# Kernel tuning notes

Measured on AMD Instinct MI355X. Metric: run time of the kernel, lower is better.

Reference implementation:

```python
import jax, jax.numpy as jnp
import numpy as np

NEG_FILL = -10000.0  # matches masked_fill_(mask, -10000.0)


def setup_inputs() -> dict:
    key0 = jax.random.key(0)
    kq, kk, kv, km = jax.random.split(key0, 4)
    B, H, S, D = 2, 16, 2048, 64
    query = jax.random.normal(kq, (B, H, S, D), dtype=jnp.float32)
    key = jax.random.normal(kk, (B, H, S, D), dtype=jnp.float32)
    value = jax.random.normal(kv, (B, H, S, D), dtype=jnp.float32)
    # key-padding mask [B, S]; True = position is masked out
    mask = jax.random.randint(km, (B, S), 0, 2).astype(jnp.bool_)
    return {"query": query, "key": key, "value": value, "mask": mask}


def reference(query, key, value, mask):
    # scaled dot-product attention: [B,H,S,D] x [B,H,S,D] -> [B,H,S,S]
    scale = 1.0 / jnp.sqrt(jnp.asarray(query.shape[-1], query.dtype))
    scores = jnp.einsum('bhqd,bhkd->bhqk', query, key) * scale
    # mask [B,S] -> broadcast over heads and query positions as [B,1,1,S]
    scores = jnp.where(mask[:, None, None, :], jnp.asarray(NEG_FILL, scores.dtype), scores)
    attn = jax.nn.softmax(scores, axis=-1)
    # dropout probs are 0 (eval-mode identity)
    out = jnp.einsum('bhqk,bhkd->bhqd', attn, value)
    return out
```

## Files before the change

kernel.cpp:

```cpp
#include <hip/hip_runtime.h>
#include <hip/hip_bf16.h>
#include <stdint.h>

namespace {

constexpr int Bb = 2;
constexpr int Hh = 16;
constexpr int Ss = 2048;
constexpr int Dd = 64;
constexpr int KT = 64;
constexpr int NT = Ss / KT;
constexpr int TILE_BYTES = KT * Dd * 2;
constexpr int BH_BYTES = NT * TILE_BYTES;
constexpr size_t KPRE_BYTES = (size_t)Bb * Hh * Ss * Dd * 2;
constexpr size_t VPRE_OFF = KPRE_BYTES;
constexpr size_t MASK_OFF = 2 * KPRE_BYTES;
constexpr size_t WS_NEED = MASK_OFF + (size_t)Bb * NT * 8;
constexpr int NIT = 16;
constexpr int IT_BYTES = 2 * TILE_BYTES;

typedef __bf16 bf16x8 __attribute__((ext_vector_type(8)));
typedef float floatx4 __attribute__((ext_vector_type(4)));

typedef __attribute__((address_space(1))) const unsigned int guint;
typedef __attribute__((address_space(3))) unsigned int luint;

__device__ __forceinline__ void g2lds16(const void* g, void* l) {
  __builtin_amdgcn_global_load_lds((guint*)g, (luint*)l, 16, 0, 0);
}

__global__ __launch_bounds__(256) void preprocess3(
    const float* __restrict__ K, const float* __restrict__ V,
    const int* __restrict__ mask, uint8_t* __restrict__ ws)
{
  const int tid = threadIdx.x;
  const int kt = blockIdx.x;
  const int bh = blockIdx.y;

  if (blockIdx.z == 0) {
    const int c = tid & 7;
#pragma unroll
    for (int half = 0; half < 2; ++half) {
      const int row = (tid >> 3) + half * 32;
      const float4* src = (const float4*)(K + ((size_t)bh * 2048 + kt * 64 + row) * 64 + c * 8);
      const float4 a = src[0], b2 = src[1];
      bf16x8 pk;
      pk[0] = (__bf16)a.x;  pk[1] = (__bf16)a.y;  pk[2] = (__bf16)a.z;  pk[3] = (__bf16)a.w;
      pk[4] = (__bf16)b2.x; pk[5] = (__bf16)b2.y; pk[6] = (__bf16)b2.z; pk[7] = (__bf16)b2.w;
      uint8_t* dst = ws + (size_t)bh * BH_BYTES + kt * TILE_BYTES + row * 128 + ((c ^ (row & 7)) << 4);
      *(bf16x8*)dst = pk;
    }
    if (bh == 0 && kt < 16) {
      const int i = kt * 256 + tid;
      const int bb = i >> 11, key = i & 2047;
      const unsigned long long bal = __ballot(mask[bb * 2048 + key] != 0);
      if ((key & 63) == 0)
        ((unsigned long long*)(ws + MASK_OFF))[bb * NT + (key >> 6)] = bal;
    }
    return;
  }

  __shared__ float Vsh[64 * 68];
#pragma unroll
  for (int i = 0; i < 4; ++i) {
    const int vt = tid + 256 * i;
    const int row = vt >> 4, c4 = vt & 15;
    const float4 v4 = *(const float4*)(V + ((size_t)bh * 2048 + kt * 64 + row) * 64 + c4 * 4);
    *(float4*)&Vsh[row * 68 + c4 * 4] = v4;
  }
  __syncthreads();
  {
    const int c16 = tid & 7;
    const int s2 = c16 & 1, q = c16 >> 1;
    const int k0 = 32 * s2 + 4 * q;
#pragma unroll
    for (int half = 0; half < 2; ++half) {
      const int d = (tid >> 3) + half * 32;
      bf16x8 pv;
#pragma unroll
      for (int j = 0; j < 4; ++j) {
        pv[j]     = (__bf16)Vsh[(k0 + j) * 68 + d];
        pv[4 + j] = (__bf16)Vsh[(k0 + 16 + j) * 68 + d];
      }
      uint8_t* dst = ws + VPRE_OFF + (size_t)bh * BH_BYTES + kt * TILE_BYTES + d * 128 + ((c16 ^ (d & 7)) << 4);
      *(bf16x8*)dst = pv;
    }
  }
}

#define NEGM (-14426.950408889634f)

__global__ __launch_bounds__(256, 2) void attn_fused6(
    const float* __restrict__ Q, const uint8_t* __restrict__ ws,
    float* __restrict__ Out)
{
  const int tid  = threadIdx.x;
  const int wave = tid >> 6;
  const int lane = tid & 63;
  const int ln   = lane & 15;
  const int quad = lane >> 4;

  const int bh   = blockIdx.x;
  const int qblk = blockIdx.y;
  const int b    = bh >> 4;

  const float* Qb = Q + (size_t)bh * Ss * Dd;
  float*       Ob = Out + (size_t)bh * Ss * Dd;
  const uint8_t* Kpre = ws + (size_t)bh * BH_BYTES;
  const uint8_t* Vpre = ws + VPRE_OFF + (size_t)bh * BH_BYTES;
  const unsigned long long* Mbits = (const unsigned long long*)(ws + MASK_OFF) + b * NT;

  __shared__ __align__(16) __bf16 Klds[2][128 * Dd];
  __shared__ __align__(16) __bf16 Vlds[2][128 * Dd];

  const int q0A = qblk * 128 + wave * 32;
  const int q0B = q0A + 16;

  const float QS = 0.125f * 1.44269504088896340736f;
  bf16x8 aqA0, aqA1, aqB0, aqB1;
  {
    const float* qpA = Qb + (size_t)(q0A + ln) * Dd + quad * 8;
    const float* qpB = Qb + (size_t)(q0B + ln) * Dd + quad * 8;
#pragma unroll
    for (int j = 0; j < 8; ++j) {
      aqA0[j] = (__bf16)(qpA[j] * QS);
      aqA1[j] = (__bf16)(qpA[32 + j] * QS);
      aqB0[j] = (__bf16)(qpB[j] * QS);
      aqB1[j] = (__bf16)(qpB[32 + j] * QS);
    }
  }

  floatx4 oA[4], oB[4];
  floatx4 laccA = (floatx4){0.f, 0.f, 0.f, 0.f};
  floatx4 laccB = (floatx4){0.f, 0.f, 0.f, 0.f};
#pragma unroll
  for (int nd = 0; nd < 4; ++nd) {
    oA[nd] = (floatx4){0.f, 0.f, 0.f, 0.f};
    oB[nd] = (floatx4){0.f, 0.f, 0.f, 0.f};
  }

  const int swz0 = (quad ^ (ln & 7)) << 4;
  const int swz1 = ((quad + 4) ^ (ln & 7)) << 4;
  const int soff = wave * 4096 + lane * 16;

#pragma unroll
  for (int i = 0; i < 4; ++i) {
    g2lds16(Kpre + soff + i * 1024, (uint8_t*)Klds[0] + soff + i * 1024);
    g2lds16(Vpre + soff + i * 1024, (uint8_t*)Vlds[0] + soff + i * 1024);
  }

  for (int kt2 = 0; kt2 < NIT; ++kt2) {
    const int cur = kt2 & 1;
    __syncthreads();

    if (kt2 + 1 < NIT) {
      const uint8_t* kg = Kpre + (kt2 + 1) * IT_BYTES;
      const uint8_t* vg = Vpre + (kt2 + 1) * IT_BYTES;
      uint8_t* kl = (uint8_t*)Klds[cur ^ 1];
      uint8_t* vl = (uint8_t*)Vlds[cur ^ 1];
#pragma unroll
      for (int i = 0; i < 4; ++i) {
        g2lds16(kg + soff + i * 1024, kl + soff + i * 1024);
        g2lds16(vg + soff + i * 1024, vl + soff + i * 1024);
      }
    }

    const unsigned long long mb0 = Mbits[2 * kt2];
    const unsigned long long mb1 = Mbits[2 * kt2 + 1];
    floatx4 biasC[8];
#pragma unroll
    for (int sub = 0; sub < 8; ++sub) {
      const unsigned long long mbx = (sub & 4) ? mb1 : mb0;
      const uint32_t bits = (uint32_t)(mbx >> ((sub & 3) * 16 + quad * 4));
#pragma unroll
      for (int r = 0; r < 4; ++r)
        biasC[sub][r] = ((bits >> r) & 1) ? NEGM : 0.f;
    }

    floatx4 sA[8], sB[8];
#pragma unroll
    for (int sub = 0; sub < 8; ++sub) {
      const uint8_t* krow = (const uint8_t*)Klds[cur] + (sub >> 2) * 8192 + ((sub & 3) * 16 + ln) * 128;
      const bf16x8 bk0 = *(const bf16x8*)(krow + swz0);
      const bf16x8 bk1 = *(const bf16x8*)(krow + swz1);
      floatx4 cA = biasC[sub];
      cA = __builtin_amdgcn_mfma_f32_16x16x32_bf16(bk0, aqA0, cA, 0, 0, 0);
      cA = __builtin_amdgcn_mfma_f32_16x16x32_bf16(bk1, aqA1, cA, 0, 0, 0);
      sA[sub] = cA;
      floatx4 cB = biasC[sub];
      cB = __builtin_amdgcn_mfma_f32_16x16x32_bf16(bk0, aqB0, cB, 0, 0, 0);
      cB = __builtin_amdgcn_mfma_f32_16x16x32_bf16(bk1, aqB1, cB, 0, 0, 0);
      sB[sub] = cB;
    }

    bf16x8 bpA[4], bpB[4];
#pragma unroll
    for (int sub = 0; sub < 8; ++sub) {
      const int pair = sub >> 1, u = sub & 1;
#pragma unroll
      for (int r = 0; r < 4; ++r) {
        const float pA = __builtin_amdgcn_exp2f(sA[sub][r]);
        const float pB = __builtin_amdgcn_exp2f(sB[sub][r]);
        laccA[r] += pA;
        laccB[r] += pB;
        bpA[pair][u * 4 + r] = (__bf16)pA;
        bpB[pair][u * 4 + r] = (__bf16)pB;
      }
    }

#pragma unroll
    for (int nd = 0; nd < 4; ++nd) {
#pragma unroll
      for (int T = 0; T < 2; ++T) {
        const uint8_t* vrow = (const uint8_t*)Vlds[cur] + T * 8192 + (nd * 16 + ln) * 128;
#pragma unroll
        for (int s2 = 0; s2 < 2; ++s2) {
          const bf16x8 w = *(const bf16x8*)(vrow + (((quad * 2 + s2) ^ (ln & 7)) << 4));
          const int pair = T * 2 + s2;
          oA[nd] = __builtin_amdgcn_mfma_f32_16x16x32_bf16(w, bpA[pair], oA[nd], 0, 0, 0);
          oB[nd] = __builtin_amdgcn_mfma_f32_16x16x32_bf16(w, bpB[pair], oB[nd], 0, 0, 0);
        }
      }
    }
  }

  float lA = (laccA[0] + laccA[1]) + (laccA[2] + laccA[3]);
  float lB = (laccB[0] + laccB[1]) + (laccB[2] + laccB[3]);
  lA += __shfl_xor(lA, 16); lA += __shfl_xor(lA, 32);
  lB += __shfl_xor(lB, 16); lB += __shfl_xor(lB, 32);
  const float iA = 1.0f / lA, iB = 1.0f / lB;
#pragma unroll
  for (int nd = 0; nd < 4; ++nd) {
    float4 wv;
    wv.x = oA[nd][0] * iA; wv.y = oA[nd][1] * iA;
    wv.z = oA[nd][2] * iA; wv.w = oA[nd][3] * iA;
    *(float4*)(Ob + (size_t)(q0A + ln) * Dd + nd * 16 + quad * 4) = wv;
    wv.x = oB[nd][0] * iB; wv.y = oB[nd][1] * iB;
    wv.z = oB[nd][2] * iB; wv.w = oB[nd][3] * iB;
    *(float4*)(Ob + (size_t)(q0B + ln) * Dd + nd * 16 + quad * 4) = wv;
  }
}

}

extern "C" void kernel_launch(void* const* d_in, const int* in_sizes, int n_in,
                              void* d_out, int out_size, void* d_ws, size_t ws_size,
                              hipStream_t stream) {
  const float* Q   = (const float*)d_in[0];
  const float* K   = (const float*)d_in[1];
  const float* V   = (const float*)d_in[2];
  const int*  mask = (const int*)d_in[3];
  float* Out = (float*)d_out;

  preprocess3<<<dim3(32, 32, 2), 256, 0, stream>>>(K, V, mask, (uint8_t*)d_ws);
  attn_fused6<<<dim3(Bb * Hh, Ss / 128), 256, 0, stream>>>(Q, (const uint8_t*)d_ws, Out);
  (void)ws_size; (void)in_sizes; (void)n_in; (void)out_size;
}
```

Measured before the change: 135.9 us.

## Process 64 query rows per wave with two-wave blocks for K/V reuse

```diff
diff --git a/kernel.cpp b/kernel.cpp
--- a/kernel.cpp
+++ b/kernel.cpp
@@ -15,7 +15,6 @@
 constexpr size_t KPRE_BYTES = (size_t)Bb * Hh * Ss * Dd * 2;
 constexpr size_t VPRE_OFF = KPRE_BYTES;
 constexpr size_t MASK_OFF = 2 * KPRE_BYTES;
-constexpr size_t WS_NEED = MASK_OFF + (size_t)Bb * NT * 8;
 constexpr int NIT = 16;
 constexpr int IT_BYTES = 2 * TILE_BYTES;
 
@@ -90,7 +89,7 @@
 
 #define NEGM (-14426.950408889634f)
 
-__global__ __launch_bounds__(256, 2) void attn_fused6(
+__global__ __launch_bounds__(128, 1) void attn_fused7(
     const float* __restrict__ Q, const uint8_t* __restrict__ ws,
     float* __restrict__ Out)
 {
@@ -113,40 +112,38 @@
   __shared__ __align__(16) __bf16 Klds[2][128 * Dd];
   __shared__ __align__(16) __bf16 Vlds[2][128 * Dd];
 
-  const int q0A = qblk * 128 + wave * 32;
-  const int q0B = q0A + 16;
+  const int qbase = qblk * 128 + wave * 64;
 
   const float QS = 0.125f * 1.44269504088896340736f;
-  bf16x8 aqA0, aqA1, aqB0, aqB1;
-  {
-    const float* qpA = Qb + (size_t)(q0A + ln) * Dd + quad * 8;
-    const float* qpB = Qb + (size_t)(q0B + ln) * Dd + quad * 8;
+  bf16x8 aq0[4], aq1[4];
+#pragma unroll
+  for (int X = 0; X < 4; ++X) {
+    const float* qp = Qb + (size_t)(qbase + X * 16 + ln) * Dd + quad * 8;
 #pragma unroll
     for (int j = 0; j < 8; ++j) {
-      aqA0[j] = (__bf16)(qpA[j] * QS);
-      aqA1[j] = (__bf16)(qpA[32 + j] * QS);
-      aqB0[j] = (__bf16)(qpB[j] * QS);
-      aqB1[j] = (__bf16)(qpB[32 + j] * QS);
-    }
-  }
-
-  floatx4 oA[4], oB[4];
-  floatx4 laccA = (floatx4){0.f, 0.f, 0.f, 0.f};
-  floatx4 laccB = (floatx4){0.f, 0.f, 0.f, 0.f};
-#pragma unroll
-  for (int nd = 0; nd < 4; ++nd) {
-    oA[nd] = (floatx4){0.f, 0.f, 0.f, 0.f};
-    oB[nd] = (floatx4){0.f, 0.f, 0.f, 0.f};
+      aq0[X][j] = (__bf16)(qp[j] * QS);
+      aq1[X][j] = (__bf16)(qp[32 + j] * QS);
+    }
+  }
+
+  floatx4 o[4][4];
+  floatx4 lacc[4];
+#pragma unroll
+  for (int X = 0; X < 4; ++X) {
+    lacc[X] = (floatx4){0.f, 0.f, 0.f, 0.f};
+#pragma unroll
+    for (int nd = 0; nd < 4; ++nd) o[X][nd] = (floatx4){0.f, 0.f, 0.f, 0.f};
   }
 
   const int swz0 = (quad ^ (ln & 7)) << 4;
   const int swz1 = ((quad + 4) ^ (ln & 7)) << 4;
-  const int soff = wave * 4096 + lane * 16;
-
-#pragma unroll
-  for (int i = 0; i < 4; ++i) {
-    g2lds16(Kpre + soff + i * 1024, (uint8_t*)Klds[0] + soff + i * 1024);
-    g2lds16(Vpre + soff + i * 1024, (uint8_t*)Vlds[0] + soff + i * 1024);
+
+  const int soff = tid * 16;
+
+#pragma unroll
+  for (int i = 0; i < 8; ++i) {
+    g2lds16(Kpre + soff + i * 2048, (uint8_t*)Klds[0] + soff + i * 2048);
+    g2lds16(Vpre + soff + i * 2048, (uint8_t*)Vlds[0] + soff + i * 2048);
   }
 
   for (int kt2 = 0; kt2 < NIT; ++kt2) {
@@ -159,85 +156,86 @@
       uint8_t* kl = (uint8_t*)Klds[cur ^ 1];
       uint8_t* vl = (uint8_t*)Vlds[cur ^ 1];
 #pragma unroll
-      for (int i = 0; i < 4; ++i) {
-        g2lds16(kg + soff + i * 1024, kl + soff + i * 1024);
-        g2lds16(vg + soff + i * 1024, vl + soff + i * 1024);
+      for (int i = 0; i < 8; ++i) {
+        g2lds16(kg + soff + i * 2048, kl + soff + i * 2048);
+        g2lds16(vg + soff + i * 2048, vl + soff + i * 2048);
       }
     }
 
     const unsigned long long mb0 = Mbits[2 * kt2];
     const unsigned long long mb1 = Mbits[2 * kt2 + 1];
-    floatx4 biasC[8];
-#pragma unroll
-    for (int sub = 0; sub < 8; ++sub) {
-      const unsigned long long mbx = (sub & 4) ? mb1 : mb0;
-      const uint32_t bits = (uint32_t)(mbx >> ((sub & 3) * 16 + quad * 4));
-#pragma unroll
-      for (int r = 0; r < 4; ++r)
-        biasC[sub][r] = ((bits >> r) & 1) ? NEGM : 0.f;
-    }
-
-    floatx4 sA[8], sB[8];
-#pragma unroll
-    for (int sub = 0; sub < 8; ++sub) {
-      const uint8_t* krow = (const uint8_t*)Klds[cur] + (sub >> 2) * 8192 + ((sub & 3) * 16 + ln) * 128;
-      const bf16x8 bk0 = *(const bf16x8*)(krow + swz0);
-      const bf16x8 bk1 = *(const bf16x8*)(krow + swz1);
-      floatx4 cA = biasC[sub];
-      cA = __builtin_amdgcn_mfma_f32_16x16x32_bf16(bk0, aqA0, cA, 0, 0, 0);
-      cA = __builtin_amdgcn_mfma_f32_16x16x32_bf16(bk1, aqA1, cA, 0, 0, 0);
-      sA[sub] = cA;
-      floatx4 cB = biasC[sub];
-      cB = __builtin_amdgcn_mfma_f32_16x16x32_bf16(bk0, aqB0, cB, 0, 0, 0);
-      cB = __builtin_amdgcn_mfma_f32_16x16x32_bf16(bk1, aqB1, cB, 0, 0, 0);
-      sB[sub] = cB;
-    }
-
-    bf16x8 bpA[4], bpB[4];
-#pragma unroll
-    for (int sub = 0; sub < 8; ++sub) {
-      const int pair = sub >> 1, u = sub & 1;
-#pragma unroll
-      for (int r = 0; r < 4; ++r) {
-        const float pA = __builtin_amdgcn_exp2f(sA[sub][r]);
-        const float pB = __builtin_amdgcn_exp2f(sB[sub][r]);
-        laccA[r] += pA;
-        laccB[r] += pB;
-        bpA[pair][u * 4 + r] = (__bf16)pA;
-        bpB[pair][u * 4 + r] = (__bf16)pB;
-      }
-    }
-
-#pragma unroll
-    for (int nd = 0; nd < 4; ++nd) {
-#pragma unroll
-      for (int T = 0; T < 2; ++T) {
+
+#pragma unroll
+    for (int T = 0; T < 2; ++T) {
+      const unsigned long long mbx = T ? mb1 : mb0;
+
+      floatx4 biasC[4];
+#pragma unroll
+      for (int s4 = 0; s4 < 4; ++s4) {
+        const uint32_t bits = (uint32_t)(mbx >> (s4 * 16 + quad * 4));
+#pragma unroll
+        for (int r = 0; r < 4; ++r)
+          biasC[s4][r] = ((bits >> r) & 1) ? NEGM : 0.f;
+      }
+
+      floatx4 s[4][4];
+#pragma unroll
+      for (int s4 = 0; s4 < 4; ++s4) {
+        const uint8_t* krow = (const uint8_t*)Klds[cur] + T * 8192 + (s4 * 16 + ln) * 128;
+        const bf16x8 bk0 = *(const bf16x8*)(krow + swz0);
+        const bf16x8 bk1 = *(const bf16x8*)(krow + swz1);
+#pragma unroll
+        for (int X = 0; X < 4; ++X) {
+          floatx4 c = biasC[s4];
+          c = __builtin_amdgcn_mfma_f32_16x16x32_bf16(bk0, aq0[X], c, 0, 0, 0);
+          c = __builtin_amdgcn_mfma_f32_16x16x32_bf16(bk1, aq1[X], c, 0, 0, 0);
+          s[s4][X] = c;
+        }
+      }
+
+      bf16x8 bp[4][2];
+#pragma unroll
+      for (int s4 = 0; s4 < 4; ++s4) {
+        const int s2 = s4 >> 1, u = s4 & 1;
+#pragma unroll
+        for (int X = 0; X < 4; ++X) {
+#pragma unroll
+          for (int r = 0; r < 4; ++r) {
+            const float p = __builtin_amdgcn_exp2f(s[s4][X][r]);
+            lacc[X][r] += p;
+            bp[X][s2][u * 4 + r] = (__bf16)p;
+          }
+        }
+      }
+
+#pragma unroll
+      for (int nd = 0; nd < 4; ++nd) {
         const uint8_t* vrow = (const uint8_t*)Vlds[cur] + T * 8192 + (nd * 16 + ln) * 128;
 #pragma unroll
         for (int s2 = 0; s2 < 2; ++s2) {
           const bf16x8 w = *(const bf16x8*)(vrow + (((quad * 2 + s2) ^ (ln & 7)) << 4));
-          const int pair = T * 2 + s2;
-          oA[nd] = __builtin_amdgcn_mfma_f32_16x16x32_bf16(w, bpA[pair], oA[nd], 0, 0, 0);
-          oB[nd] = __builtin_amdgcn_mfma_f32_16x16x32_bf16(w, bpB[pair], oB[nd], 0, 0, 0);
+#pragma unroll
+          for (int X = 0; X < 4; ++X)
+            o[X][nd] = __builtin_amdgcn_mfma_f32_16x16x32_bf16(w, bp[X][s2], o[X][nd], 0, 0, 0);
         }
       }
     }
   }
 
-  float lA = (laccA[0] + laccA[1]) + (laccA[2] + laccA[3]);
-  float lB = (laccB[0] + laccB[1]) + (laccB[2] + laccB[3]);
-  lA += __shfl_xor(lA, 16); lA += __shfl_xor(lA, 32);
-  lB += __shfl_xor(lB, 16); lB += __shfl_xor(lB, 32);
-  const float iA = 1.0f / lA, iB = 1.0f / lB;
-#pragma unroll
-  for (int nd = 0; nd < 4; ++nd) {
-    float4 wv;
-    wv.x = oA[nd][0] * iA; wv.y = oA[nd][1] * iA;
-    wv.z = oA[nd][2] * iA; wv.w = oA[nd][3] * iA;
-    *(float4*)(Ob + (size_t)(q0A + ln) * Dd + nd * 16 + quad * 4) = wv;
-    wv.x = oB[nd][0] * iB; wv.y = oB[nd][1] * iB;
-    wv.z = oB[nd][2] * iB; wv.w = oB[nd][3] * iB;
-    *(float4*)(Ob + (size_t)(q0B + ln) * Dd + nd * 16 + quad * 4) = wv;
+#pragma unroll
+  for (int X = 0; X < 4; ++X) {
+    float l = (lacc[X][0] + lacc[X][1]) + (lacc[X][2] + lacc[X][3]);
+    l += __shfl_xor(l, 16);
+    l += __shfl_xor(l, 32);
+    const float inv = 1.0f / l;
+    float* obX = Ob + (size_t)(qbase + X * 16 + ln) * Dd;
+#pragma unroll
+    for (int nd = 0; nd < 4; ++nd) {
+      float4 wv;
+      wv.x = o[X][nd][0] * inv; wv.y = o[X][nd][1] * inv;
+      wv.z = o[X][nd][2] * inv; wv.w = o[X][nd][3] * inv;
+      *(float4*)(obX + nd * 16 + quad * 4) = wv;
+    }
   }
 }
 
@@ -253,6 +251,6 @@
   float* Out = (float*)d_out;
 
   preprocess3<<<dim3(32, 32, 2), 256, 0, stream>>>(K, V, mask, (uint8_t*)d_ws);
-  attn_fused6<<<dim3(Bb * Hh, Ss / 128), 256, 0, stream>>>(Q, (const uint8_t*)d_ws, Out);
+  attn_fused7<<<dim3(Bb * Hh, Ss / 128), 128, 0, stream>>>(Q, (const uint8_t*)d_ws, Out);
   (void)ws_size; (void)in_sizes; (void)n_in; (void)out_size;
 }
```

Result: slower. 145.2 us (+6.8%).

## Halve key tile per iteration, raise occupancy, compute row sums via MFMA

Applied to the files above, without the earlier changes.

```diff
diff --git a/kernel.cpp b/kernel.cpp
--- a/kernel.cpp
+++ b/kernel.cpp
@@ -15,9 +15,6 @@
 constexpr size_t KPRE_BYTES = (size_t)Bb * Hh * Ss * Dd * 2;
 constexpr size_t VPRE_OFF = KPRE_BYTES;
 constexpr size_t MASK_OFF = 2 * KPRE_BYTES;
-constexpr size_t WS_NEED = MASK_OFF + (size_t)Bb * NT * 8;
-constexpr int NIT = 16;
-constexpr int IT_BYTES = 2 * TILE_BYTES;
 
 typedef __bf16 bf16x8 __attribute__((ext_vector_type(8)));
 typedef float floatx4 __attribute__((ext_vector_type(4)));
@@ -90,7 +87,7 @@
 
 #define NEGM (-14426.950408889634f)
 
-__global__ __launch_bounds__(256, 2) void attn_fused6(
+__global__ __launch_bounds__(256, 4) void attn_fused8(
     const float* __restrict__ Q, const uint8_t* __restrict__ ws,
     float* __restrict__ Out)
 {
@@ -110,8 +107,8 @@
   const uint8_t* Vpre = ws + VPRE_OFF + (size_t)bh * BH_BYTES;
   const unsigned long long* Mbits = (const unsigned long long*)(ws + MASK_OFF) + b * NT;
 
-  __shared__ __align__(16) __bf16 Klds[2][128 * Dd];
-  __shared__ __align__(16) __bf16 Vlds[2][128 * Dd];
+  __shared__ __align__(16) __bf16 Klds[2][KT * Dd];
+  __shared__ __align__(16) __bf16 Vlds[2][KT * Dd];
 
   const int q0A = qblk * 128 + wave * 32;
   const int q0B = q0A + 16;
@@ -130,9 +127,13 @@
     }
   }
 
+  bf16x8 ones;
+#pragma unroll
+  for (int j = 0; j < 8; ++j) ones[j] = (__bf16)1.0f;
+
   floatx4 oA[4], oB[4];
-  floatx4 laccA = (floatx4){0.f, 0.f, 0.f, 0.f};
-  floatx4 laccB = (floatx4){0.f, 0.f, 0.f, 0.f};
+  floatx4 clA = (floatx4){0.f, 0.f, 0.f, 0.f};
+  floatx4 clB = (floatx4){0.f, 0.f, 0.f, 0.f};
 #pragma unroll
   for (int nd = 0; nd < 4; ++nd) {
     oA[nd] = (floatx4){0.f, 0.f, 0.f, 0.f};
@@ -141,46 +142,43 @@
 
   const int swz0 = (quad ^ (ln & 7)) << 4;
   const int swz1 = ((quad + 4) ^ (ln & 7)) << 4;
-  const int soff = wave * 4096 + lane * 16;
-
-#pragma unroll
-  for (int i = 0; i < 4; ++i) {
-    g2lds16(Kpre + soff + i * 1024, (uint8_t*)Klds[0] + soff + i * 1024);
-    g2lds16(Vpre + soff + i * 1024, (uint8_t*)Vlds[0] + soff + i * 1024);
-  }
-
-  for (int kt2 = 0; kt2 < NIT; ++kt2) {
-    const int cur = kt2 & 1;
+  const int soff0 = wave * 2048 + lane * 16;
+  const int soff1 = soff0 + 1024;
+
+  g2lds16(Kpre + soff0, (uint8_t*)Klds[0] + soff0);
+  g2lds16(Vpre + soff0, (uint8_t*)Vlds[0] + soff0);
+  g2lds16(Kpre + soff1, (uint8_t*)Klds[0] + soff1);
+  g2lds16(Vpre + soff1, (uint8_t*)Vlds[0] + soff1);
+
+  for (int kt = 0; kt < NT; ++kt) {
+    const int cur = kt & 1;
     __syncthreads();
 
-    if (kt2 + 1 < NIT) {
-      const uint8_t* kg = Kpre + (kt2 + 1) * IT_BYTES;
-      const uint8_t* vg = Vpre + (kt2 + 1) * IT_BYTES;
+    if (kt + 1 < NT) {
+      const uint8_t* kg = Kpre + (kt + 1) * TILE_BYTES;
+      const uint8_t* vg = Vpre + (kt + 1) * TILE_BYTES;
       uint8_t* kl = (uint8_t*)Klds[cur ^ 1];
       uint8_t* vl = (uint8_t*)Vlds[cur ^ 1];
-#pragma unroll
-      for (int i = 0; i < 4; ++i) {
-        g2lds16(kg + soff + i * 1024, kl + soff + i * 1024);
-        g2lds16(vg + soff + i * 1024, vl + soff + i * 1024);
-      }
-    }
-
-    const unsigned long long mb0 = Mbits[2 * kt2];
-    const unsigned long long mb1 = Mbits[2 * kt2 + 1];
-    floatx4 biasC[8];
-#pragma unroll
-    for (int sub = 0; sub < 8; ++sub) {
-      const unsigned long long mbx = (sub & 4) ? mb1 : mb0;
-      const uint32_t bits = (uint32_t)(mbx >> ((sub & 3) * 16 + quad * 4));
+      g2lds16(kg + soff0, kl + soff0);
+      g2lds16(vg + soff0, vl + soff0);
+      g2lds16(kg + soff1, kl + soff1);
+      g2lds16(vg + soff1, vl + soff1);
+    }
+
+    const unsigned long long mb = Mbits[kt];
+    floatx4 biasC[4];
+#pragma unroll
+    for (int sub = 0; sub < 4; ++sub) {
+      const uint32_t bits = (uint32_t)(mb >> (sub * 16 + quad * 4));
 #pragma unroll
       for (int r = 0; r < 4; ++r)
         biasC[sub][r] = ((bits >> r) & 1) ? NEGM : 0.f;
     }
 
-    floatx4 sA[8], sB[8];
-#pragma unroll
-    for (int sub = 0; sub < 8; ++sub) {
-      const uint8_t* krow = (const uint8_t*)Klds[cur] + (sub >> 2) * 8192 + ((sub & 3) * 16 + ln) * 128;
+    floatx4 sA[4], sB[4];
+#pragma unroll
+    for (int sub = 0; sub < 4; ++sub) {
+      const uint8_t* krow = (const uint8_t*)Klds[cur] + (sub * 16 + ln) * 128;
       const bf16x8 bk0 = *(const bf16x8*)(krow + swz0);
       const bf16x8 bk1 = *(const bf16x8*)(krow + swz1);
       floatx4 cA = biasC[sub];
@@ -193,42 +191,36 @@
       sB[sub] = cB;
     }
 
-    bf16x8 bpA[4], bpB[4];
-#pragma unroll
-    for (int sub = 0; sub < 8; ++sub) {
-      const int pair = sub >> 1, u = sub & 1;
+    bf16x8 bpA[2], bpB[2];
+#pragma unroll
+    for (int sub = 0; sub < 4; ++sub) {
+      const int s2 = sub >> 1, u = sub & 1;
 #pragma unroll
       for (int r = 0; r < 4; ++r) {
-        const float pA = __builtin_amdgcn_exp2f(sA[sub][r]);
-        const float pB = __builtin_amdgcn_exp2f(sB[sub][r]);
-        laccA[r] += pA;
-        laccB[r] += pB;
-        bpA[pair][u * 4 + r] = (__bf16)pA;
-        bpB[pair][u * 4 + r] = (__bf16)pB;
+        bpA[s2][u * 4 + r] = (__bf16)__builtin_amdgcn_exp2f(sA[sub][r]);
+        bpB[s2][u * 4 + r] = (__bf16)__builtin_amdgcn_exp2f(sB[sub][r]);
       }
     }
 
+    clA = __builtin_amdgcn_mfma_f32_16x16x32_bf16(ones, bpA[0], clA, 0, 0, 0);
+    clA = __builtin_amdgcn_mfma_f32_16x16x32_bf16(ones, bpA[1], clA, 0, 0, 0);
+    clB = __builtin_amdgcn_mfma_f32_16x16x32_bf16(ones, bpB[0], clB, 0, 0, 0);
+    clB = __builtin_amdgcn_mfma_f32_16x16x32_bf16(ones, bpB[1], clB, 0, 0, 0);
+
 #pragma unroll
     for (int nd = 0; nd < 4; ++nd) {
-#pragma unroll
-      for (int T = 0; T < 2; ++T) {
-        const uint8_t* vrow = (const uint8_t*)Vlds[cur] + T * 8192 + (nd * 16 + ln) * 128;
-#pragma unroll
-        for (int s2 = 0; s2 < 2; ++s2) {
-          const bf16x8 w = *(const bf16x8*)(vrow + (((quad * 2 + s2) ^ (ln & 7)) << 4));
-          const int pair = T * 2 + s2;
-          oA[nd] = __builtin_amdgcn_mfma_f32_16x16x32_bf16(w, bpA[pair], oA[nd], 0, 0, 0);
-          oB[nd] = __builtin_amdgcn_mfma_f32_16x16x32_bf16(w, bpB[pair], oB[nd], 0, 0, 0);
-        }
+      const uint8_t* vrow = (const uint8_t*)Vlds[cur] + (nd * 16 + ln) * 128;
+#pragma unroll
+      for (int s2 = 0; s2 < 2; ++s2) {
+        const bf16x8 w = *(const bf16x8*)(vrow + (((quad * 2 + s2) ^ (ln & 7)) << 4));
+        oA[nd] = __builtin_amdgcn_mfma_f32_16x16x32_bf16(w, bpA[s2], oA[nd], 0, 0, 0);
+        oB[nd] = __builtin_amdgcn_mfma_f32_16x16x32_bf16(w, bpB[s2], oB[nd], 0, 0, 0);
       }
     }
   }
 
-  float lA = (laccA[0] + laccA[1]) + (laccA[2] + laccA[3]);
-  float lB = (laccB[0] + laccB[1]) + (laccB[2] + laccB[3]);
-  lA += __shfl_xor(lA, 16); lA += __shfl_xor(lA, 32);
-  lB += __shfl_xor(lB, 16); lB += __shfl_xor(lB, 32);
-  const float iA = 1.0f / lA, iB = 1.0f / lB;
+  const float iA = 1.0f / clA[0];
+  const float iB = 1.0f / clB[0];
 #pragma unroll
   for (int nd = 0; nd < 4; ++nd) {
     float4 wv;
@@ -253,6 +245,6 @@
   float* Out = (float*)d_out;
 
   preprocess3<<<dim3(32, 32, 2), 256, 0, stream>>>(K, V, mask, (uint8_t*)d_ws);
-  attn_fused6<<<dim3(Bb * Hh, Ss / 128), 256, 0, stream>>>(Q, (const uint8_t*)d_ws, Out);
+  attn_fused8<<<dim3(Bb * Hh, Ss / 128), 256, 0, stream>>>(Q, (const uint8_t*)d_ws, Out);
   (void)ws_size; (void)in_sizes; (void)n_in; (void)out_size;
 }
```

Result: no change. 136.1 us (+0.1%).
